# Kernel optimization log

Hardware: AMD Instinct MI355X
Metric: run time of the kernel (lower is better)

## Reference

```python
import jax, jax.numpy as jnp
import numpy as np

BZ, C, H, W = 8, 512, 64, 64


def setup_inputs() -> dict:
    key = jax.random.key(0)
    x = jax.random.normal(key, (BZ, C, H, W), dtype=jnp.float32)
    # central square hole: flag==1 -> masked (unknown), flag==0 -> known
    mask = np.zeros((H, W), dtype=np.int32)
    mask[H // 4: 3 * H // 4, W // 4: 3 * W // 4] = 1
    return {"x": x, "mask": jnp.asarray(mask)}


def reference(x, mask):
    # InnerShiftSingle forward with shift_sz=1, stride=1, mask_thred=1:
    # flag == feature-level mask (each 1x1 patch is masked iff its pixel is masked).
    bz, c, h, w = x.shape
    c2 = c // 2
    hw = h * w
    flag = mask.reshape(hw)  # [hw] int, 1=masked, 0=known

    former = x[:, :c2]   # decoder features [b,c2,h,w]
    latter = x[:, c2:]   # encoder features [b,c2,h,w]

    former_f = former.reshape(bz, c2, hw).transpose(0, 2, 1)  # [b,hw,c2]
    latter_f = latter.reshape(bz, c2, hw).transpose(0, 2, 1)  # [b,hw,c2]

    # original: conv of (un-normalized) former with L2-normalized latter 1x1 patches
    latter_n = latter_f / (jnp.linalg.norm(latter_f, axis=-1, keepdims=True) + 1e-8)
    cosine = jnp.einsum('bpc,bqc->bpq', former_f, latter_n)  # [b,hw,hw]
    # only known-region patches (flag==0) are candidate sources
    cosine = jnp.where(flag[None, None, :] == 1, -jnp.inf, cosine)

    best = jnp.argmax(cosine, axis=-1)  # [b,hw] index into known region
    shift = jnp.take_along_axis(latter_f, best[..., None], axis=1)  # [b,hw,c2]
    # only masked positions receive a shifted feature; known positions stay 0
    shift = jnp.where(flag[None, :, None] == 1, shift, jnp.zeros((), x.dtype))
    shift = shift.transpose(0, 2, 1).reshape(bz, c2, h, w)

    return jnp.concatenate([former, latter, shift], axis=1)  # [b, 3c/2, h, w]
```

## Files before the change

kernel.cpp:

```cpp
#include <hip/hip_runtime.h>
#include <math.h>

#define BZc 8
#define Cc 512
#define C2c 256
#define HWc 4096
#define OUTC 768
#define NP 1024
#define NQ 3072
#define QG 8
#define TAU 5e-5f
#define FIXSLOTS 64

typedef _Float16 h8 __attribute__((ext_vector_type(8)));
typedef float f16v __attribute__((ext_vector_type(16)));
typedef float f32x4 __attribute__((ext_vector_type(4)));

__global__ __launch_bounds__(1024) void k_build(const int* __restrict__ mask,
                                                int* __restrict__ pidx,
                                                int* __restrict__ qinv,
                                                int* __restrict__ pinv,
                                                int* __restrict__ cnt) {
    __shared__ int s0[1024], s1[1024], t0[1024], t1[1024];
    int t = threadIdx.x;
    if (t < 8) cnt[t] = 0;
    int f[4];
    int cp = 0;
#pragma unroll
    for (int j = 0; j < 4; ++j) { f[j] = mask[t * 4 + j]; cp += f[j]; }
    s0[t] = cp; s1[t] = 4 - cp;
    __syncthreads();
    int *a = s0, *b = s1, *c = t0, *d = t1;
    for (int off = 1; off < 1024; off <<= 1) {
        int vp = a[t] + (t >= off ? a[t - off] : 0);
        int vq = b[t] + (t >= off ? b[t - off] : 0);
        c[t] = vp; d[t] = vq;
        __syncthreads();
        int* tmp;
        tmp = a; a = c; c = tmp;
        tmp = b; b = d; d = tmp;
    }
    int ep = a[t] - cp;
    int eq = b[t] - (4 - cp);
#pragma unroll
    for (int j = 0; j < 4; ++j) {
        int idx = t * 4 + j;
        if (f[j]) { pidx[ep] = idx; pinv[idx] = ep; qinv[idx] = -1; ep++; }
        else      { qinv[idx] = eq; pinv[idx] = -1; eq++; }
    }
}

__global__ __launch_bounds__(256) void k_prep(const float* __restrict__ x,
                                              const int* __restrict__ pinv,
                                              const int* __restrict__ qinv,
                                              _Float16* __restrict__ latH,
                                              _Float16* __restrict__ latL,
                                              _Float16* __restrict__ forH,
                                              _Float16* __restrict__ forL,
                                              float* __restrict__ invn,
                                              float* __restrict__ invnC,
                                              float* __restrict__ out) {
    int id = blockIdx.x;
    bool isLat = id < 512;
    int b = isLat ? (id >> 6) : ((id - 512) >> 6);
    int g = isLat ? (id & 63) : ((id - 512) & 63);
    int tid = threadIdx.x;
    __shared__ float tile[64][65];
    __shared__ float ssq[16][65];
    __shared__ int rowm[64];
    if (tid < 64) rowm[tid] = isLat ? qinv[g * 64 + tid] : pinv[g * 64 + tid];
    __syncthreads();
    const float* xb = x + (size_t)b * Cc * HWc + (isLat ? (size_t)C2c * HWc : 0);
    float* ob = out + (size_t)b * OUTC * HWc + (isLat ? (size_t)C2c * HWc : 0);
    _Float16* dH = isLat ? latH + (size_t)b * NQ * 256 : forH + (size_t)b * NP * 256;
    _Float16* dL = isLat ? latL + (size_t)b * NQ * 256 : forL + (size_t)b * NP * 256;

    int cr = tid >> 4;
    int c4 = (tid & 15) * 4;
    float s0 = 0.f, s1 = 0.f, s2 = 0.f, s3 = 0.f;

    for (int c0 = 0; c0 < 256; c0 += 64) {
#pragma unroll
        for (int p = 0; p < 4; ++p) {
            int lch = p * 16 + cr;
            int ch = c0 + lch;
            const f32x4 v = *(const f32x4*)(xb + (size_t)ch * HWc + g * 64 + c4);
            __builtin_nontemporal_store(v, (f32x4*)(ob + (size_t)ch * HWc + g * 64 + c4));
            if (isLat) {
                s0 = fmaf(v.x, v.x, s0); s1 = fmaf(v.y, v.y, s1);
                s2 = fmaf(v.z, v.z, s2); s3 = fmaf(v.w, v.w, s3);
            }
            tile[lch][c4]     = v.x;
            tile[lch][c4 + 1] = v.y;
            tile[lch][c4 + 2] = v.z;
            tile[lch][c4 + 3] = v.w;
        }
        __syncthreads();
        int qq = tid >> 2, sub = tid & 3;
        int dr = rowm[qq];
        if (dr >= 0) {
            h8 hv0, hv1, lv0, lv1;
#pragma unroll
            for (int j = 0; j < 8; ++j) {
                float v = tile[sub * 16 + j][qq];
                _Float16 h = (_Float16)v;
                hv0[j] = h; lv0[j] = (_Float16)((v - (float)h) * 2048.0f);
            }
#pragma unroll
            for (int j = 0; j < 8; ++j) {
                float v = tile[sub * 16 + 8 + j][qq];
                _Float16 h = (_Float16)v;
                hv1[j] = h; lv1[j] = (_Float16)((v - (float)h) * 2048.0f);
            }
            size_t o = (size_t)dr * 256 + c0 + sub * 16;
            *(h8*)(dH + o) = hv0; *(h8*)(dH + o + 8) = hv1;
            *(h8*)(dL + o) = lv0; *(h8*)(dL + o + 8) = lv1;
        }
        __syncthreads();
    }
    if (isLat) {
        ssq[cr][c4] = s0; ssq[cr][c4 + 1] = s1; ssq[cr][c4 + 2] = s2; ssq[cr][c4 + 3] = s3;
        __syncthreads();
        if (tid < 64) {
            float s = 0.f;
#pragma unroll
            for (int r = 0; r < 16; ++r) s += ssq[r][tid];
            float inv = 1.0f / (sqrtf(s) + 1e-8f);
            int q = g * 64 + tid;
            invn[b * HWc + q] = inv;
            int qc = rowm[tid];
            if (qc >= 0) invnC[b * NQ + qc] = inv;
        }
    } else {
        f32x4 z = {0.f, 0.f, 0.f, 0.f};
        float* sb = out + (size_t)b * OUTC * HWc + (size_t)Cc * HWc;
        for (int i = tid; i < 256 * 16; i += 256) {
            int ch = i >> 4, j4 = i & 15;
            __builtin_nontemporal_store(z, (f32x4*)(sb + (size_t)ch * HWc + g * 64 + j4 * 4));
        }
    }
}

__global__ __launch_bounds__(512, 2) void k_gemm(const _Float16* __restrict__ latH,
                                                 const _Float16* __restrict__ latL,
                                                 const _Float16* __restrict__ forH,
                                                 const _Float16* __restrict__ forL,
                                                 const float* __restrict__ invnC,
                                                 float* __restrict__ bv1,
                                                 int* __restrict__ bi1,
                                                 float* __restrict__ bv2) {
    int pg = blockIdx.x;
    int qg = blockIdx.y;
    int b  = blockIdx.z;
    int tid = threadIdx.x;
    int w = tid >> 6, lane = tid & 63;
    int l31 = lane & 31, lh = lane >> 5;

    __shared__ __align__(16) _Float16 sH[2][32 * 256];
    __shared__ __align__(16) _Float16 sL[2][32 * 256];
    __shared__ float sInv[384];

    if (tid < 384) sInv[tid] = invnC[b * NQ + qg * 384 + tid];

    size_t fo = ((size_t)(b * NP + pg * 256 + w * 32 + l31)) * 256 + lh * 8;
    const _Float16* fH = forH + fo;
    const _Float16* fL = forL + fo;
    h8 BH[16], BL[16];
#pragma unroll
    for (int ks = 0; ks < 16; ++ks) {
        BH[ks] = *(const h8*)(fH + ks * 16);
        BL[ks] = *(const h8*)(fL + ks * 16);
    }

    const _Float16* latHb = latH + (size_t)(b * NQ + qg * 384) * 256;
    const _Float16* latLb = latL + (size_t)(b * NQ + qg * 384) * 256;
    int sq0 = tid >> 5;
    int sq1 = 16 + (tid >> 5);
    int ssl = tid & 31;

    float v1 = -INFINITY, v2 = -INFINITY; int i1 = 0;

    f32x4 rH0, rH1, rL0, rL1;
#define LOADQ(t)                                                                   \
    rH0 = *(const f32x4*)(latHb + ((size_t)((t) * 32 + sq0) * 256 + ssl * 8));     \
    rH1 = *(const f32x4*)(latHb + ((size_t)((t) * 32 + sq1) * 256 + ssl * 8));     \
    rL0 = *(const f32x4*)(latLb + ((size_t)((t) * 32 + sq0) * 256 + ssl * 8));     \
    rL1 = *(const f32x4*)(latLb + ((size_t)((t) * 32 + sq1) * 256 + ssl * 8));
#define WRITEQ(bf)                                                                 \
    *(f32x4*)(&sH[bf][sq0 * 256 + ((ssl ^ sq0) * 8)]) = rH0;                       \
    *(f32x4*)(&sH[bf][sq1 * 256 + ((ssl ^ sq1) * 8)]) = rH1;                       \
    *(f32x4*)(&sL[bf][sq0 * 256 + ((ssl ^ sq0) * 8)]) = rL0;                       \
    *(f32x4*)(&sL[bf][sq1 * 256 + ((ssl ^ sq1) * 8)]) = rL1;

    LOADQ(0); WRITEQ(0);
    __syncthreads();

    for (int t = 0; t < 12; ++t) {
        if (t < 11) { LOADQ(t + 1); }
        const _Float16* bufH = &sH[t & 1][0];
        const _Float16* bufL = &sL[t & 1][0];
        f16v accA = {}, accB = {};
#pragma unroll
        for (int ks = 0; ks < 16; ++ks) {
            int slotA = (ks * 2 + lh) ^ l31;
            h8 aH = *(const h8*)(bufH + l31 * 256 + slotA * 8);
            h8 aL = *(const h8*)(bufL + l31 * 256 + slotA * 8);
            accA = __builtin_amdgcn_mfma_f32_32x32x16_f16(aH, BH[ks], accA, 0, 0, 0);
            accB = __builtin_amdgcn_mfma_f32_32x32x16_f16(aH, BL[ks], accB, 0, 0, 0);
            accB = __builtin_amdgcn_mfma_f32_32x32x16_f16(aL, BH[ks], accB, 0, 0, 0);
        }
#pragma unroll
        for (int r = 0; r < 16; ++r) {
            int off = (r & 3) + 8 * (r >> 2) + 4 * lh;
            float v = (accA[r] + accB[r] * (1.0f / 2048.0f)) * sInv[t * 32 + off];
            int q = qg * 384 + t * 32 + off;
            if (v > v1) { v2 = v1; v1 = v; i1 = q; }
            else if (v > v2) { v2 = v; }
        }
        if (t < 11) { WRITEQ((t + 1) & 1); }
        __syncthreads();
    }
#undef LOADQ
#undef WRITEQ
    float ov1 = __shfl_xor(v1, 32);
    int   oi1 = __shfl_xor(i1, 32);
    float ov2 = __shfl_xor(v2, 32);
    if (ov1 > v1) { v2 = fmaxf(v1, ov2); v1 = ov1; i1 = oi1; }
    else          { v2 = fmaxf(ov1, v2); }
    if (lane < 32) {
        size_t o = ((size_t)b * NP + pg * 256 + w * 32 + lane) * QG + qg;
        bv1[o] = v1; bi1[o] = i1; bv2[o] = v2;
    }
}

__global__ void k_reduce(const float* __restrict__ bv1, const int* __restrict__ bi1,
                         const float* __restrict__ bv2, int* __restrict__ bfin,
                         int* __restrict__ cnt, int* __restrict__ fixrows) {
    int t = blockIdx.x * blockDim.x + threadIdx.x;
    if (t >= BZc * NP) return;
    float V1 = -INFINITY, V2 = -INFINITY; int I1 = 0;
    for (int c = 0; c < QG; ++c) {
        float a = bv1[(size_t)t * QG + c];
        float a2 = bv2[(size_t)t * QG + c];
        int   i = bi1[(size_t)t * QG + c];
        if (a > V1) { V2 = fmaxf(V1, a2); V1 = a; I1 = i; }
        else        { V2 = fmaxf(V2, a); }
    }
    bfin[t] = I1;
    if (V1 - V2 < TAU) {
        int b = t >> 10;
        int s = atomicAdd(&cnt[b], 1);
        if (s < FIXSLOTS) fixrows[b * FIXSLOTS + s] = t & 1023;
    }
}

__global__ __launch_bounds__(256) void k_fixA(const float* __restrict__ x,
                                              const int* __restrict__ pidx,
                                              const int* __restrict__ mask,
                                              const float* __restrict__ invn,
                                              const int* __restrict__ cnt,
                                              const int* __restrict__ fixrows,
                                              float* __restrict__ fixv,
                                              int* __restrict__ fixi) {
    int qg = blockIdx.x, s = blockIdx.y, b = blockIdx.z;
    int n = cnt[b]; if (n > FIXSLOTS) n = FIXSLOTS;
    if (s >= n) return;
    int p = fixrows[b * FIXSLOTS + s];
    int porig = pidx[p];
    int tid = threadIdx.x;
    __shared__ float fs[256];
    fs[tid] = x[((size_t)b * Cc + tid) * HWc + porig];
    __syncthreads();
    const float* lx = x + ((size_t)b * Cc + C2c) * HWc;
    int q0 = qg * 1024 + tid * 4;
    float4 acc = make_float4(0.f, 0.f, 0.f, 0.f);
    for (int c0 = 0; c0 < 256; c0 += 8) {
        float4 v[8];
#pragma unroll
        for (int u = 0; u < 8; ++u)
            v[u] = *(const float4*)(lx + (size_t)(c0 + u) * HWc + q0);
#pragma unroll
        for (int u = 0; u < 8; ++u) {
            float fc = fs[c0 + u];
            acc.x = fmaf(fc, v[u].x, acc.x);
            acc.y = fmaf(fc, v[u].y, acc.y);
            acc.z = fmaf(fc, v[u].z, acc.z);
            acc.w = fmaf(fc, v[u].w, acc.w);
        }
    }
    float vals[4] = {acc.x, acc.y, acc.z, acc.w};
    float bv = -INFINITY; int bq = 1 << 30;
#pragma unroll
    for (int k = 0; k < 4; ++k) {
        int q = q0 + k;
        float val = vals[k] * invn[b * HWc + q];
        if (mask[q] == 0 && val > bv) { bv = val; bq = q; }
    }
    __shared__ float rv[256]; __shared__ int rq[256];
    rv[tid] = bv; rq[tid] = bq; __syncthreads();
    for (int off = 128; off > 0; off >>= 1) {
        if (tid < off) {
            float v2 = rv[tid + off]; int q2 = rq[tid + off];
            if (v2 > rv[tid] || (v2 == rv[tid] && q2 < rq[tid])) { rv[tid] = v2; rq[tid] = q2; }
        }
        __syncthreads();
    }
    if (tid == 0) {
        fixv[(b * FIXSLOTS + s) * 4 + qg] = rv[0];
        fixi[(b * FIXSLOTS + s) * 4 + qg] = rq[0];
    }
}

__global__ void k_fixB(const int* __restrict__ cnt, const int* __restrict__ fixrows,
                       const float* __restrict__ fixv, const int* __restrict__ fixi,
                       const int* __restrict__ qinv, int* __restrict__ bfin) {
    int t = threadIdx.x;
    int b = t >> 6, s = t & 63;
    int n = cnt[b]; if (n > FIXSLOTS) n = FIXSLOTS;
    if (s >= n) return;
    float bv = -INFINITY; int bq = 1 << 30;
    for (int qg = 0; qg < 4; ++qg) {
        float v = fixv[(b * FIXSLOTS + s) * 4 + qg];
        int   q = fixi[(b * FIXSLOTS + s) * 4 + qg];
        if (v > bv || (v == bv && q < bq)) { bv = v; bq = q; }
    }
    int p = fixrows[b * FIXSLOTS + s];
    bfin[b * NP + p] = qinv[bq];
}

__global__ __launch_bounds__(256) void k_scatter(const _Float16* __restrict__ latH,
                                                 const _Float16* __restrict__ latL,
                                                 const int* __restrict__ bfin,
                                                 const int* __restrict__ pidx,
                                                 float* __restrict__ out) {
    int blk = blockIdx.x;
    int b   = blockIdx.y;
    int tid = threadIdx.x;
    __shared__ float tile[32][257];
    __shared__ int qd[32], pd[32];
    if (tid < 32) {
        qd[tid] = bfin[b * NP + blk * 32 + tid];
        pd[tid] = pidx[blk * 32 + tid];
    }
    __syncthreads();
    for (int i = tid; i < 32 * 256; i += 256) {
        int pp = i >> 8, c = i & 255;
        size_t o = ((size_t)b * NQ + qd[pp]) * 256 + c;
        tile[pp][c] = (float)latH[o] + (float)latL[o] * (1.0f / 2048.0f);
    }
    __syncthreads();
    float* ob = out + (size_t)b * OUTC * HWc + (size_t)Cc * HWc;
    for (int i = tid; i < 256 * 32; i += 256) {
        int ch = i >> 5, j = i & 31;
        ob[(size_t)ch * HWc + pd[j]] = tile[j][ch];
    }
}

extern "C" void kernel_launch(void* const* d_in, const int* in_sizes, int n_in,
                              void* d_out, int out_size, void* d_ws, size_t ws_size,
                              hipStream_t stream) {
    const float* x    = (const float*)d_in[0];
    const int*   mask = (const int*)d_in[1];
    float* out = (float*)d_out;
    char*  ws  = (char*)d_ws;

    _Float16* latH = (_Float16*)(ws);
    _Float16* latL = (_Float16*)(ws + 12582912);
    _Float16* forH = (_Float16*)(ws + 25165824);
    _Float16* forL = (_Float16*)(ws + 29360128);
    float* invn    = (float*)(ws + 33554432);
    float* invnC   = (float*)(ws + 33685504);
    float* bv1     = (float*)(ws + 33783808);
    int*   bi1     = (int*)  (ws + 34045952);
    float* bv2     = (float*)(ws + 34308096);
    int*   bfin    = (int*)  (ws + 34570240);
    int*   pidx    = (int*)  (ws + 34603008);
    int*   qinv    = (int*)  (ws + 34607104);
    int*   pinv    = (int*)  (ws + 34623488);
    int*   cnt     = (int*)  (ws + 34639872);
    int*   fixrows = (int*)  (ws + 34639904);
    float* fixv    = (float*)(ws + 34641952);
    int*   fixi    = (int*)  (ws + 34650144);

    k_build<<<1, 1024, 0, stream>>>(mask, pidx, qinv, pinv, cnt);
    k_prep<<<1024, 256, 0, stream>>>(x, pinv, qinv, latH, latL, forH, forL, invn, invnC, out);
    k_gemm<<<dim3(4, QG, BZc), 512, 0, stream>>>(latH, latL, forH, forL, invnC, bv1, bi1, bv2);
    k_reduce<<<(BZc * NP + 255) / 256, 256, 0, stream>>>(bv1, bi1, bv2, bfin, cnt, fixrows);
    k_fixA<<<dim3(4, FIXSLOTS, BZc), 256, 0, stream>>>(x, pidx, mask, invn, cnt, fixrows, fixv, fixi);
    k_fixB<<<1, 512, 0, stream>>>(cnt, fixrows, fixv, fixi, qinv, bfin);
    k_scatter<<<dim3(32, BZc), 256, 0, stream>>>(latH, latL, bfin, pidx, out);
}
```

Measured before the change: 113.2 us.

## Halve prep tile width, double grid, and prefetch next channel chunk into registers

The prep kernel now handles 32 spatial columns per block instead of 64, which doubles the grid to 2048 blocks. It keeps all 256 channel values in registers and loads the next 64-channel chunk while the current shared-memory tile is being converted to fp16 hi/lo. The passthrough copy stores and the norm accumulation are moved after the loop and read from those registers. This is meant to give more parallelism and overlap global loads with the transpose work, at the cost of more registers per thread and narrower 128-byte row segments per load.

```diff
diff --git a/kernel.cpp b/kernel.cpp
--- a/kernel.cpp
+++ b/kernel.cpp
@@ -61,82 +61,95 @@
                                               float* __restrict__ invnC,
                                               float* __restrict__ out) {
     int id = blockIdx.x;
-    bool isLat = id < 512;
-    int b = isLat ? (id >> 6) : ((id - 512) >> 6);
-    int g = isLat ? (id & 63) : ((id - 512) & 63);
+    bool isLat = id < 1024;
+    int rid = isLat ? id : id - 1024;
+    int b = rid >> 7;
+    int g = rid & 127;
+    int col0 = g * 32;
     int tid = threadIdx.x;
-    __shared__ float tile[64][65];
-    __shared__ float ssq[16][65];
-    __shared__ int rowm[64];
-    if (tid < 64) rowm[tid] = isLat ? qinv[g * 64 + tid] : pinv[g * 64 + tid];
-    __syncthreads();
+    __shared__ float tile[64][33];
+    __shared__ float ssq[32][33];
+    __shared__ int rowm[32];
+    if (tid < 32) rowm[tid] = isLat ? qinv[col0 + tid] : pinv[col0 + tid];
     const float* xb = x + (size_t)b * Cc * HWc + (isLat ? (size_t)C2c * HWc : 0);
     float* ob = out + (size_t)b * OUTC * HWc + (isLat ? (size_t)C2c * HWc : 0);
     _Float16* dH = isLat ? latH + (size_t)b * NQ * 256 : forH + (size_t)b * NP * 256;
     _Float16* dL = isLat ? latL + (size_t)b * NQ * 256 : forL + (size_t)b * NP * 256;
 
-    int cr = tid >> 4;
-    int c4 = (tid & 15) * 4;
-    float s0 = 0.f, s1 = 0.f, s2 = 0.f, s3 = 0.f;
-
-    for (int c0 = 0; c0 < 256; c0 += 64) {
-#pragma unroll
-        for (int p = 0; p < 4; ++p) {
-            int lch = p * 16 + cr;
-            int ch = c0 + lch;
-            const f32x4 v = *(const f32x4*)(xb + (size_t)ch * HWc + g * 64 + c4);
-            __builtin_nontemporal_store(v, (f32x4*)(ob + (size_t)ch * HWc + g * 64 + c4));
-            if (isLat) {
+    int cr = tid >> 3;
+    int c4 = (tid & 7) * 4;
+
+    f32x4 vv[4][2];
+    vv[0][0] = *(const f32x4*)(xb + (size_t)cr * HWc + col0 + c4);
+    vv[0][1] = *(const f32x4*)(xb + (size_t)(32 + cr) * HWc + col0 + c4);
+    __syncthreads();
+
+    int qq = tid >> 3, sub = tid & 7;
+    int dr = rowm[qq];
+
+#pragma unroll
+    for (int c = 0; c < 4; ++c) {
+        int ch0 = c * 64;
+        {
+            f32x4 v0 = vv[c][0], v1 = vv[c][1];
+            tile[cr][c4]      = v0.x; tile[cr][c4 + 1]      = v0.y;
+            tile[cr][c4 + 2]  = v0.z; tile[cr][c4 + 3]      = v0.w;
+            tile[32 + cr][c4] = v1.x; tile[32 + cr][c4 + 1] = v1.y;
+            tile[32 + cr][c4 + 2] = v1.z; tile[32 + cr][c4 + 3] = v1.w;
+        }
+        __syncthreads();
+        if (c < 3) {
+            vv[c + 1][0] = *(const f32x4*)(xb + (size_t)(ch0 + 64 + cr) * HWc + col0 + c4);
+            vv[c + 1][1] = *(const f32x4*)(xb + (size_t)(ch0 + 96 + cr) * HWc + col0 + c4);
+        }
+        if (dr >= 0) {
+            h8 hv, lv;
+#pragma unroll
+            for (int j = 0; j < 8; ++j) {
+                float v = tile[sub * 8 + j][qq];
+                _Float16 h = (_Float16)v;
+                hv[j] = h; lv[j] = (_Float16)((v - (float)h) * 2048.0f);
+            }
+            size_t o = (size_t)dr * 256 + ch0 + sub * 8;
+            *(h8*)(dH + o) = hv;
+            *(h8*)(dL + o) = lv;
+        }
+        __syncthreads();
+    }
+
+#pragma unroll
+    for (int c = 0; c < 4; ++c) {
+        __builtin_nontemporal_store(vv[c][0], (f32x4*)(ob + (size_t)(c * 64 + cr) * HWc + col0 + c4));
+        __builtin_nontemporal_store(vv[c][1], (f32x4*)(ob + (size_t)(c * 64 + 32 + cr) * HWc + col0 + c4));
+    }
+
+    if (isLat) {
+        float s0 = 0.f, s1 = 0.f, s2 = 0.f, s3 = 0.f;
+#pragma unroll
+        for (int c = 0; c < 4; ++c)
+#pragma unroll
+            for (int p = 0; p < 2; ++p) {
+                f32x4 v = vv[c][p];
                 s0 = fmaf(v.x, v.x, s0); s1 = fmaf(v.y, v.y, s1);
                 s2 = fmaf(v.z, v.z, s2); s3 = fmaf(v.w, v.w, s3);
             }
-            tile[lch][c4]     = v.x;
-            tile[lch][c4 + 1] = v.y;
-            tile[lch][c4 + 2] = v.z;
-            tile[lch][c4 + 3] = v.w;
-        }
-        __syncthreads();
-        int qq = tid >> 2, sub = tid & 3;
-        int dr = rowm[qq];
-        if (dr >= 0) {
-            h8 hv0, hv1, lv0, lv1;
-#pragma unroll
-            for (int j = 0; j < 8; ++j) {
-                float v = tile[sub * 16 + j][qq];
-                _Float16 h = (_Float16)v;
-                hv0[j] = h; lv0[j] = (_Float16)((v - (float)h) * 2048.0f);
-            }
-#pragma unroll
-            for (int j = 0; j < 8; ++j) {
-                float v = tile[sub * 16 + 8 + j][qq];
-                _Float16 h = (_Float16)v;
-                hv1[j] = h; lv1[j] = (_Float16)((v - (float)h) * 2048.0f);
-            }
-            size_t o = (size_t)dr * 256 + c0 + sub * 16;
-            *(h8*)(dH + o) = hv0; *(h8*)(dH + o + 8) = hv1;
-            *(h8*)(dL + o) = lv0; *(h8*)(dL + o + 8) = lv1;
-        }
-        __syncthreads();
-    }
-    if (isLat) {
         ssq[cr][c4] = s0; ssq[cr][c4 + 1] = s1; ssq[cr][c4 + 2] = s2; ssq[cr][c4 + 3] = s3;
         __syncthreads();
-        if (tid < 64) {
+        if (tid < 32) {
             float s = 0.f;
 #pragma unroll
-            for (int r = 0; r < 16; ++r) s += ssq[r][tid];
+            for (int r = 0; r < 32; ++r) s += ssq[r][tid];
             float inv = 1.0f / (sqrtf(s) + 1e-8f);
-            int q = g * 64 + tid;
-            invn[b * HWc + q] = inv;
+            invn[b * HWc + col0 + tid] = inv;
             int qc = rowm[tid];
             if (qc >= 0) invnC[b * NQ + qc] = inv;
         }
     } else {
         f32x4 z = {0.f, 0.f, 0.f, 0.f};
         float* sb = out + (size_t)b * OUTC * HWc + (size_t)Cc * HWc;
-        for (int i = tid; i < 256 * 16; i += 256) {
-            int ch = i >> 4, j4 = i & 15;
-            __builtin_nontemporal_store(z, (f32x4*)(sb + (size_t)ch * HWc + g * 64 + j4 * 4));
+        for (int i = tid; i < 256 * 8; i += 256) {
+            int ch = i >> 3, j4 = i & 7;
+            __builtin_nontemporal_store(z, (f32x4*)(sb + (size_t)ch * HWc + col0 + j4 * 4));
         }
     }
 }
@@ -383,7 +396,7 @@
     int*   fixi    = (int*)  (ws + 34650144);
 
     k_build<<<1, 1024, 0, stream>>>(mask, pidx, qinv, pinv, cnt);
-    k_prep<<<1024, 256, 0, stream>>>(x, pinv, qinv, latH, latL, forH, forL, invn, invnC, out);
+    k_prep<<<2048, 256, 0, stream>>>(x, pinv, qinv, latH, latL, forH, forL, invn, invnC, out);
     k_gemm<<<dim3(4, QG, BZc), 512, 0, stream>>>(latH, latL, forH, forL, invnC, bv1, bi1, bv2);
     k_reduce<<<(BZc * NP + 255) / 256, 256, 0, stream>>>(bv1, bi1, bv2, bfin, cnt, fixrows);
     k_fixA<<<dim3(4, FIXSLOTS, BZc), 256, 0, stream>>>(x, pidx, mask, invn, cnt, fixrows, fixv, fixi);
```

Measured after the change: 112.1 us. No clear change (-1.0%).
